# Kernel optimization log

Measured on AMD Instinct MI355X. Metric: run time of the kernel, lower is better.

Reference implementation:

```python
import jax, jax.numpy as jnp
import numpy as np

H = 8          # num_heads
D = 64         # out_dim per head
ROT = D // 2   # rotary dim per spatial axis (out_dim // relative_emb_dim)
MIN_FREQ = 1.0 / 64


def _freqs(t):
    # t: (bs, N) coordinates -> (bs, N, ROT)
    inv_freq = 1.0 / (10000.0 ** (jnp.arange(0, ROT, 2, dtype=jnp.float32) / ROT))
    f = (t / MIN_FREQ)[..., None] * inv_freq  # (bs, N, ROT/2)
    return jnp.concatenate([f, f], axis=-1)   # (bs, N, ROT)


def _rotate_half(x):
    x1, x2 = jnp.split(x, 2, axis=-1)
    return jnp.concatenate([-x2, x1], axis=-1)


def _rope(t, f):
    return t * jnp.cos(f) + _rotate_half(t) * jnp.sin(f)


def reference(h, pos, Wq, Wk, Wv, src, dst):
    bs, N, _ = pos.shape
    hb = h.reshape(bs, N, -1)                       # (bs, N, C)
    # Faithful to torch: Linear output (bs,N,H*D) .view(bs,H,N,D) is a raw
    # memory reinterpretation, i.e. a reshape, not a transpose.
    Qh = (hb @ Wq.T).reshape(bs, H, N, D)
    Kh = (hb @ Wk.T).reshape(bs, H, N, D)
    Vh = (hb @ Wv.T).reshape(bs, H, N, D)

    fx = _freqs(pos[..., 0])[:, None]               # (bs, 1, N, ROT) broadcast over heads
    fy = _freqs(pos[..., 1])[:, None]

    def rope2d(t):
        return jnp.concatenate([_rope(t[..., :ROT], fx), _rope(t[..., ROT:], fy)], axis=-1)

    Qh = rope2d(Qh)
    Kh = rope2d(Kh)

    Qn = Qh.reshape(-1, H, D)                       # (bs*N, H, D) flat node layout
    Kn = Kh.reshape(-1, H, D)
    Vn = Vh.reshape(-1, H, D)

    # edge attention: gather, dot, clamped exp, scatter-sum
    score = jnp.sum(Kn[src] * Qn[dst], axis=-1)     # (E, H)
    score = jnp.exp(jnp.clip(score / np.sqrt(D).astype(np.float32), -5.0, 5.0))

    nseg = bs * N
    wV = jax.ops.segment_sum(Vn[src] * score[..., None], dst, num_segments=nseg)  # (nseg,H,D)
    z = jax.ops.segment_sum(score, dst, num_segments=nseg)                        # (nseg,H)

    attn_out = wV / z[..., None]
    return attn_out.reshape(-1, H * D)


def setup_inputs() -> dict:
    key = jax.random.key(0)
    k = jax.random.split(key, 7)
    bs, N, C, E = 4, 4096, 256, 524288
    return {
        "h": jax.random.normal(k[0], (bs * N, C), dtype=jnp.float32),
        "pos": jax.random.uniform(k[1], (bs, N, 2), dtype=jnp.float32),
        "Wq": jax.random.normal(k[2], (H * D, C), dtype=jnp.float32) * 0.05,
        "Wk": jax.random.normal(k[3], (H * D, C), dtype=jnp.float32) * 0.05,
        "Wv": jax.random.normal(k[4], (H * D, C), dtype=jnp.float32) * 0.05,
        "src": jax.random.randint(k[5], (E,), 0, bs * N, dtype=jnp.int32),
        "dst": jax.random.randint(k[6], (E,), 0, bs * N, dtype=jnp.int32),
    }
```

## Files before the change

kernel.cpp:

```cpp
#include <hip/hip_runtime.h>
#include <math.h>

#define NODES 16384
#define CIN   256
#define HD    512
#define NPOS  4096
#define NHEAD 8
#define DDIM  64
#define HN    (NODES * CIN)
#define WN    (HD * CIN)

typedef float f32x4 __attribute__((ext_vector_type(4)));
typedef unsigned int u32x4 __attribute__((ext_vector_type(4)));
typedef short s16x8 __attribute__((ext_vector_type(8)));

__device__ inline unsigned short f2bf(float f) {
  unsigned int u = __float_as_uint(f);
  u += 0x7fffu + ((u >> 16) & 1u);
  return (unsigned short)(u >> 16);
}

__global__ __launch_bounds__(256) void conv_rank_kernel(
    const float* __restrict__ h, const float* __restrict__ wq,
    const float* __restrict__ wk, const float* __restrict__ wv,
    unsigned short* __restrict__ out,
    const int* __restrict__ dst, int* __restrict__ count,
    int* __restrict__ rank, int E) {
  int t = blockIdx.x * 256 + threadIdx.x;
  if (t < E) rank[t] = atomicAdd(&count[dst[t]], 1);

  size_t e = (size_t)t * 8;
  const float* s;
  size_t off;
  if (e < HN)               { s = h;  off = e; }
  else if (e < HN + WN)     { s = wq; off = e - HN; }
  else if (e < HN + 2 * WN) { s = wk; off = e - HN - WN; }
  else                      { s = wv; off = e - HN - 2 * WN; }
  float4 f0 = *(const float4*)(s + off);
  float4 f1 = *(const float4*)(s + off + 4);
  u32x4 o;
  o[0] = f2bf(f0.x) | ((unsigned int)f2bf(f0.y) << 16);
  o[1] = f2bf(f0.z) | ((unsigned int)f2bf(f0.w) << 16);
  o[2] = f2bf(f1.x) | ((unsigned int)f2bf(f1.y) << 16);
  o[3] = f2bf(f1.z) | ((unsigned int)f2bf(f1.w) << 16);
  *(u32x4*)(out + e) = o;
}

__global__ __launch_bounds__(256) void scan_kernel(
    const int* __restrict__ count, int* __restrict__ offset) {
  __shared__ int psum[256];
  __shared__ int pref[256];
  int t = threadIdx.x;
  int base = t * (NODES / 256);
  int s = 0;
  for (int i = 0; i < NODES / 256; ++i) s += count[base + i];
  psum[t] = s;
  __syncthreads();
  if (t < 64) {
    int a0 = psum[4 * t], a1 = psum[4 * t + 1];
    int a2 = psum[4 * t + 2], a3 = psum[4 * t + 3];
    int loc = a0 + a1 + a2 + a3;
    int sc = loc;
#pragma unroll
    for (int d = 1; d < 64; d <<= 1) {
      int v = __shfl_up(sc, d);
      if (t >= d) sc += v;
    }
    int excl = sc - loc;
    pref[4 * t]     = excl;
    pref[4 * t + 1] = excl + a0;
    pref[4 * t + 2] = excl + a0 + a1;
    pref[4 * t + 3] = excl + a0 + a1 + a2;
  }
  __syncthreads();
  int off = pref[t];
  for (int i = 0; i < NODES / 256; ++i) {
    offset[base + i] = off;
    off += count[base + i];
  }
  if (t == 255) offset[NODES] = off;
}

__global__ __launch_bounds__(256) void place_kernel(
    const int* __restrict__ src, const int* __restrict__ dst,
    const int* __restrict__ offset, const int* __restrict__ rank,
    int* __restrict__ srcs, int E) {
  int t = blockIdx.x * 256 + threadIdx.x;
  if (t < E) srcs[offset[dst[t]] + rank[t]] = src[t];
}

__global__ __launch_bounds__(256) void gemm_mfma_kernel(
    const unsigned short* __restrict__ hb,
    const unsigned short* __restrict__ wb,
    const float* __restrict__ pos,
    unsigned short* __restrict__ Qb, unsigned short* __restrict__ Kb,
    unsigned short* __restrict__ Vb) {
  const int z = blockIdx.z;
  const unsigned short* B = wb + (size_t)z * WN;
  unsigned short* C = z == 0 ? Qb : (z == 1 ? Kb : Vb);

  __shared__ __align__(16) unsigned short As[2][128 * 32];
  __shared__ __align__(16) unsigned short Bs[2][128 * 32];

  const int tid = threadIdx.x;
  const int lane = tid & 63, w = tid >> 6;
  const int row0 = blockIdx.y * 128, col0 = blockIdx.x * 128;
  const int wr = w >> 1, wc = w & 1;

  const int r_l = lane >> 2;
  const int kc = (lane & 3) * 8;

  f32x4 acc[4][4] = {};

#define STAGE(bufi, kt)                                                        \
  {                                                                            \
    _Pragma("unroll") for (int u = 0; u < 2; ++u) {                            \
      int blk = u * 4 + w;                                                     \
      int r = blk * 16 + r_l;                                                  \
      __builtin_amdgcn_global_load_lds(                                        \
          (const __attribute__((address_space(1))) void*)(hb +                 \
              (size_t)(row0 + r) * CIN + (kt) + kc),                           \
          (__attribute__((address_space(3))) void*)(&As[bufi][blk * 512]),     \
          16, 0, 0);                                                           \
      __builtin_amdgcn_global_load_lds(                                        \
          (const __attribute__((address_space(1))) void*)(B +                  \
              (size_t)(col0 + r) * CIN + (kt) + kc),                           \
          (__attribute__((address_space(3))) void*)(&Bs[bufi][blk * 512]),     \
          16, 0, 0);                                                           \
    }                                                                          \
  }

  STAGE(0, 0);
  __syncthreads();

  int cur = 0;
  for (int t = 0; t < 8; ++t) {
    if (t < 7) STAGE(cur ^ 1, (t + 1) * 32);

    s16x8 af[4], bfr[4];
#pragma unroll
    for (int mi = 0; mi < 4; ++mi)
      af[mi] = *(const s16x8*)(&As[cur][(wr * 64 + mi * 16 + (lane & 15)) * 32 + (lane >> 4) * 8]);
#pragma unroll
    for (int ni = 0; ni < 4; ++ni)
      bfr[ni] = *(const s16x8*)(&Bs[cur][(wc * 64 + ni * 16 + (lane & 15)) * 32 + (lane >> 4) * 8]);
#pragma unroll
    for (int mi = 0; mi < 4; ++mi)
#pragma unroll
      for (int ni = 0; ni < 4; ++ni)
        acc[mi][ni] = __builtin_amdgcn_mfma_f32_16x16x32_bf16(
            af[mi], bfr[ni], acc[mi][ni], 0, 0, 0);

    __syncthreads();
    cur ^= 1;
  }
#undef STAGE

  const int head = blockIdx.x * 2 + wc;
  const int cb = col0 + wc * 64 + (lane & 15);
  const float invf = exp2f(-(float)(lane & 15) * 0.83048202372184f);

#pragma unroll
  for (int mi = 0; mi < 4; ++mi) {
#pragma unroll
    for (int r = 0; r < 4; ++r) {
      int row = row0 + wr * 64 + mi * 16 + (lane >> 4) * 4 + r;
      float v0 = acc[mi][0][r], v1 = acc[mi][1][r];
      float v2 = acc[mi][2][r], v3 = acc[mi][3][r];
      if (z < 2) {
        int b = row >> 12;
        int rem = ((row & 4095) << 3) + head;
        int n = rem & (NPOS - 1);
        const float* pp = pos + ((size_t)((b << 12) + n)) * 2;
        float a0 = pp[0] * 64.0f * invf;
        float a1 = pp[1] * 64.0f * invf;
        float s0, c0, s1, c1;
        sincosf(a0, &s0, &c0);
        sincosf(a1, &s1, &c1);
        float nx0 = v0 * c0 - v1 * s0;
        float nx1 = v1 * c0 + v0 * s0;
        float ny0 = v2 * c1 - v3 * s1;
        float ny1 = v3 * c1 + v2 * s1;
        v0 = nx0; v1 = nx1; v2 = ny0; v3 = ny1;
      }
      unsigned short* cp = C + (size_t)row * HD + cb;
      cp[0]  = f2bf(v0);
      cp[16] = f2bf(v1);
      cp[32] = f2bf(v2);
      cp[48] = f2bf(v3);
    }
  }
}

__global__ __launch_bounds__(256) void node_kernel(
    const unsigned short* __restrict__ Qb, const unsigned short* __restrict__ Kb,
    const unsigned short* __restrict__ Vb,
    const int* __restrict__ srcs, const int* __restrict__ offset,
    float* __restrict__ out) {
  __shared__ float wv[4][HD];
  __shared__ float zb[4][NHEAD];
  const int n = blockIdx.x;
  const int tid = threadIdx.x;
  const int lane = tid & 63, w = tid >> 6;
  const int hh = lane >> 3, g = lane & 7;

  const int beg = offset[n], end = offset[n + 1];

  u32x4 qu = *(const u32x4*)(Qb + (size_t)n * HD + lane * 8);
  float qf[8];
#pragma unroll
  for (int j = 0; j < 4; ++j) {
    qf[2 * j]     = __uint_as_float(qu[j] << 16);
    qf[2 * j + 1] = __uint_as_float(qu[j] & 0xffff0000u);
  }

  float a[8] = {0, 0, 0, 0, 0, 0, 0, 0};
  float zacc = 0.f;

  for (int i = beg + w; i < end; i += 4) {
    int s = srcs[i];
    u32x4 ku = *(const u32x4*)(Kb + (size_t)s * HD + lane * 8);
    u32x4 vu = *(const u32x4*)(Vb + (size_t)s * HD + lane * 8);
    float dot = 0.f;
#pragma unroll
    for (int j = 0; j < 4; ++j) {
      dot += __uint_as_float(ku[j] << 16) * qf[2 * j];
      dot += __uint_as_float(ku[j] & 0xffff0000u) * qf[2 * j + 1];
    }
    dot += __shfl_xor(dot, 1);
    dot += __shfl_xor(dot, 2);
    dot += __shfl_xor(dot, 4);
    float sc = __expf(fminf(fmaxf(dot * 0.125f, -5.0f), 5.0f));
#pragma unroll
    for (int j = 0; j < 4; ++j) {
      a[2 * j]     += __uint_as_float(vu[j] << 16) * sc;
      a[2 * j + 1] += __uint_as_float(vu[j] & 0xffff0000u) * sc;
    }
    zacc += sc;
  }

  *(float4*)&wv[w][lane * 8]     = make_float4(a[0], a[1], a[2], a[3]);
  *(float4*)&wv[w][lane * 8 + 4] = make_float4(a[4], a[5], a[6], a[7]);
  if (g == 0) zb[w][hh] = zacc;
  __syncthreads();

  const int d0 = tid * 2;
  float r0 = wv[0][d0] + wv[1][d0] + wv[2][d0] + wv[3][d0];
  float r1 = wv[0][d0 + 1] + wv[1][d0 + 1] + wv[2][d0 + 1] + wv[3][d0 + 1];
  const int head = d0 >> 6;
  float zz = zb[0][head] + zb[1][head] + zb[2][head] + zb[3][head];
  float inv = 1.0f / zz;
  *(float2*)&out[(size_t)n * HD + d0] = make_float2(r0 * inv, r1 * inv);
}

extern "C" void kernel_launch(void* const* d_in, const int* in_sizes, int n_in,
                              void* d_out, int out_size, void* d_ws,
                              size_t ws_size, hipStream_t stream) {
  const float* h   = (const float*)d_in[0];
  const float* pos = (const float*)d_in[1];
  const float* Wq  = (const float*)d_in[2];
  const float* Wk  = (const float*)d_in[3];
  const float* Wv  = (const float*)d_in[4];
  const int* src   = (const int*)d_in[5];
  const int* dst   = (const int*)d_in[6];
  const int E = in_sizes[5];

  unsigned short* hb  = (unsigned short*)d_ws;
  unsigned short* wb  = hb + HN;
  unsigned short* Qb  = wb + 3 * WN;
  unsigned short* Kb  = Qb + (size_t)NODES * HD;
  unsigned short* Vb  = Kb + (size_t)NODES * HD;
  int* count  = (int*)(Vb + (size_t)NODES * HD);
  int* offset = count + NODES;
  int* rank   = offset + NODES + 1;
  int* srcs   = rank + E;
  float* out = (float*)d_out;

  hipMemsetAsync(count, 0, NODES * sizeof(int), stream);

  conv_rank_kernel<<<(HN + 3 * WN) / 8 / 256, 256, 0, stream>>>(
      h, Wq, Wk, Wv, hb, dst, count, rank, E);

  scan_kernel<<<1, 256, 0, stream>>>(count, offset);
  place_kernel<<<(E + 255) / 256, 256, 0, stream>>>(
      src, dst, offset, rank, srcs, E);

  gemm_mfma_kernel<<<dim3(HD / 128, NODES / 128, 3), 256, 0, stream>>>(
      hb, wb, pos, Qb, Kb, Vb);

  node_kernel<<<NODES, 256, 0, stream>>>(Qb, Kb, Vb, srcs, offset, out);
}
```

Before: 284.5 us.

## Store Q/K/V head-major and split node aggregation per head

The GEMM epilogue now writes Q, K and V in a head-major layout (head, node, 64), so each head's data is contiguous. The node kernel launches a 2D grid of node groups by heads, with one wave per (node, head). Two edges are handled per iteration using half-waves, which removes the shared-memory reduction and the block barrier. The aim is better cache locality, since each head's working set (16384×64 bf16) is small enough to stay resident. In exchange, edge indices and offsets are re-read once per head, and nodes with uneven edge counts cause more load imbalance and shorter per-wave loads.

```diff
diff --git a/kernel.cpp b/kernel.cpp
--- a/kernel.cpp
+++ b/kernel.cpp
@@ -157,8 +157,8 @@
 #undef STAGE
 
   const int head = blockIdx.x * 2 + wc;
-  const int cb = col0 + wc * 64 + (lane & 15);
   const float invf = exp2f(-(float)(lane & 15) * 0.83048202372184f);
+  unsigned short* Ch = C + (size_t)head * (NODES * DDIM) + (lane & 15);
 
 #pragma unroll
   for (int mi = 0; mi < 4; ++mi) {
@@ -183,7 +183,7 @@
         float ny1 = v3 * c1 + v2 * s1;
         v0 = nx0; v1 = nx1; v2 = ny0; v3 = ny1;
       }
-      unsigned short* cp = C + (size_t)row * HD + cb;
+      unsigned short* cp = Ch + (size_t)row * DDIM;
       cp[0]  = f2bf(v0);
       cp[16] = f2bf(v1);
       cp[32] = f2bf(v2);
@@ -197,60 +197,50 @@
     const unsigned short* __restrict__ Vb,
     const int* __restrict__ srcs, const int* __restrict__ offset,
     float* __restrict__ out) {
-  __shared__ float wv[4][HD];
-  __shared__ float zb[4][NHEAD];
-  const int n = blockIdx.x;
-  const int tid = threadIdx.x;
-  const int lane = tid & 63, w = tid >> 6;
-  const int hh = lane >> 3, g = lane & 7;
+  const int w = threadIdx.x >> 6, lane = threadIdx.x & 63;
+  const int n = blockIdx.x * 4 + w;
+  const int hh = blockIdx.y;
+  const int el = lane >> 5, dl = lane & 31;
+
+  const unsigned short* Qh = Qb + (size_t)hh * (NODES * DDIM);
+  const unsigned short* Kh = Kb + (size_t)hh * (NODES * DDIM);
+  const unsigned short* Vh = Vb + (size_t)hh * (NODES * DDIM);
 
   const int beg = offset[n], end = offset[n + 1];
 
-  u32x4 qu = *(const u32x4*)(Qb + (size_t)n * HD + lane * 8);
-  float qf[8];
-#pragma unroll
-  for (int j = 0; j < 4; ++j) {
-    qf[2 * j]     = __uint_as_float(qu[j] << 16);
-    qf[2 * j + 1] = __uint_as_float(qu[j] & 0xffff0000u);
-  }
-
-  float a[8] = {0, 0, 0, 0, 0, 0, 0, 0};
-  float zacc = 0.f;
-
-  for (int i = beg + w; i < end; i += 4) {
-    int s = srcs[i];
-    u32x4 ku = *(const u32x4*)(Kb + (size_t)s * HD + lane * 8);
-    u32x4 vu = *(const u32x4*)(Vb + (size_t)s * HD + lane * 8);
-    float dot = 0.f;
-#pragma unroll
-    for (int j = 0; j < 4; ++j) {
-      dot += __uint_as_float(ku[j] << 16) * qf[2 * j];
-      dot += __uint_as_float(ku[j] & 0xffff0000u) * qf[2 * j + 1];
-    }
+  unsigned int qu = __builtin_nontemporal_load(
+      (const unsigned int*)(Qh + (size_t)n * DDIM + dl * 2));
+  float q0 = __uint_as_float(qu << 16);
+  float q1 = __uint_as_float(qu & 0xffff0000u);
+
+  float a0 = 0.f, a1 = 0.f, zacc = 0.f;
+
+  for (int i = beg; i + el < end; i += 2) {
+    int s = __builtin_nontemporal_load(&srcs[i + el]);
+    unsigned int ku = *(const unsigned int*)(Kh + (size_t)s * DDIM + dl * 2);
+    float dot = __uint_as_float(ku << 16) * q0 +
+                __uint_as_float(ku & 0xffff0000u) * q1;
     dot += __shfl_xor(dot, 1);
     dot += __shfl_xor(dot, 2);
     dot += __shfl_xor(dot, 4);
+    dot += __shfl_xor(dot, 8);
+    dot += __shfl_xor(dot, 16);
     float sc = __expf(fminf(fmaxf(dot * 0.125f, -5.0f), 5.0f));
-#pragma unroll
-    for (int j = 0; j < 4; ++j) {
-      a[2 * j]     += __uint_as_float(vu[j] << 16) * sc;
-      a[2 * j + 1] += __uint_as_float(vu[j] & 0xffff0000u) * sc;
-    }
+    unsigned int vu = *(const unsigned int*)(Vh + (size_t)s * DDIM + dl * 2);
+    a0 += __uint_as_float(vu << 16) * sc;
+    a1 += __uint_as_float(vu & 0xffff0000u) * sc;
     zacc += sc;
   }
 
-  *(float4*)&wv[w][lane * 8]     = make_float4(a[0], a[1], a[2], a[3]);
-  *(float4*)&wv[w][lane * 8 + 4] = make_float4(a[4], a[5], a[6], a[7]);
-  if (g == 0) zb[w][hh] = zacc;
-  __syncthreads();
-
-  const int d0 = tid * 2;
-  float r0 = wv[0][d0] + wv[1][d0] + wv[2][d0] + wv[3][d0];
-  float r1 = wv[0][d0 + 1] + wv[1][d0 + 1] + wv[2][d0 + 1] + wv[3][d0 + 1];
-  const int head = d0 >> 6;
-  float zz = zb[0][head] + zb[1][head] + zb[2][head] + zb[3][head];
-  float inv = 1.0f / zz;
-  *(float2*)&out[(size_t)n * HD + d0] = make_float2(r0 * inv, r1 * inv);
+  a0 += __shfl_xor(a0, 32);
+  a1 += __shfl_xor(a1, 32);
+  zacc += __shfl_xor(zacc, 32);
+
+  if (lane < 32) {
+    float inv = 1.0f / zacc;
+    *(float2*)(out + (size_t)n * HD + hh * DDIM + dl * 2) =
+        make_float2(a0 * inv, a1 * inv);
+  }
 }
 
 extern "C" void kernel_launch(void* const* d_in, const int* in_sizes, int n_in,
@@ -288,5 +278,6 @@
   gemm_mfma_kernel<<<dim3(HD / 128, NODES / 128, 3), 256, 0, stream>>>(
       hb, wb, pos, Qb, Kb, Vb);
 
-  node_kernel<<<NODES, 256, 0, stream>>>(Qb, Kb, Vb, srcs, offset, out);
-}
+  node_kernel<<<dim3(NODES / 4, NHEAD), 256, 0, stream>>>(
+      Qb, Kb, Vb, srcs, offset, out);
+}
```

After: 445.9 us. 1.57x slower.

## Store Q/K/V head-major and split node aggregation per head across wavefronts

Applied to the files above, without the earlier changes.

The GEMM epilogue now writes Q, K and V in a head-major layout (head, node, 64), so each head's data is contiguous. The node kernel launches one wavefront per (node, head): 8 edges are processed in parallel with 8 lanes each, and the partial sums are reduced with shuffles instead of a shared-memory reduction and block barrier. This targets better cache locality for the gathered K/V rows within a head and removes LDS and sync overhead. In exchange it adds masked lanes for nodes whose edge counts are not multiples of 8, and the srcs indices are reloaded once per head.

```diff
diff --git a/kernel.cpp b/kernel.cpp
--- a/kernel.cpp
+++ b/kernel.cpp
@@ -157,8 +157,8 @@
 #undef STAGE
 
   const int head = blockIdx.x * 2 + wc;
-  const int cb = col0 + wc * 64 + (lane & 15);
   const float invf = exp2f(-(float)(lane & 15) * 0.83048202372184f);
+  unsigned short* Ch = C + (size_t)head * (NODES * DDIM) + (lane & 15);
 
 #pragma unroll
   for (int mi = 0; mi < 4; ++mi) {
@@ -183,7 +183,7 @@
         float ny1 = v3 * c1 + v2 * s1;
         v0 = nx0; v1 = nx1; v2 = ny0; v3 = ny1;
       }
-      unsigned short* cp = C + (size_t)row * HD + cb;
+      unsigned short* cp = Ch + (size_t)row * DDIM;
       cp[0]  = f2bf(v0);
       cp[16] = f2bf(v1);
       cp[32] = f2bf(v2);
@@ -197,16 +197,18 @@
     const unsigned short* __restrict__ Vb,
     const int* __restrict__ srcs, const int* __restrict__ offset,
     float* __restrict__ out) {
-  __shared__ float wv[4][HD];
-  __shared__ float zb[4][NHEAD];
-  const int n = blockIdx.x;
-  const int tid = threadIdx.x;
-  const int lane = tid & 63, w = tid >> 6;
-  const int hh = lane >> 3, g = lane & 7;
+  const int w = threadIdx.x >> 6, lane = threadIdx.x & 63;
+  const int n = blockIdx.x * 4 + w;
+  const int hh = blockIdx.y;
+  const int e8 = lane >> 3, d8 = lane & 7;
+
+  const unsigned short* Qh = Qb + (size_t)hh * (NODES * DDIM);
+  const unsigned short* Kh = Kb + (size_t)hh * (NODES * DDIM);
+  const unsigned short* Vh = Vb + (size_t)hh * (NODES * DDIM);
 
   const int beg = offset[n], end = offset[n + 1];
 
-  u32x4 qu = *(const u32x4*)(Qb + (size_t)n * HD + lane * 8);
+  u32x4 qu = *(const u32x4*)(Qh + (size_t)n * DDIM + d8 * 8);
   float qf[8];
 #pragma unroll
   for (int j = 0; j < 4; ++j) {
@@ -217,10 +219,12 @@
   float a[8] = {0, 0, 0, 0, 0, 0, 0, 0};
   float zacc = 0.f;
 
-  for (int i = beg + w; i < end; i += 4) {
-    int s = srcs[i];
-    u32x4 ku = *(const u32x4*)(Kb + (size_t)s * HD + lane * 8);
-    u32x4 vu = *(const u32x4*)(Vb + (size_t)s * HD + lane * 8);
+  for (int it = beg; it < end; it += 8) {
+    int e = it + e8;
+    bool ok = e < end;
+    int s = __builtin_nontemporal_load(&srcs[ok ? e : beg]);
+    u32x4 ku = *(const u32x4*)(Kh + (size_t)s * DDIM + d8 * 8);
+    u32x4 vu = *(const u32x4*)(Vh + (size_t)s * DDIM + d8 * 8);
     float dot = 0.f;
 #pragma unroll
     for (int j = 0; j < 4; ++j) {
@@ -230,7 +234,7 @@
     dot += __shfl_xor(dot, 1);
     dot += __shfl_xor(dot, 2);
     dot += __shfl_xor(dot, 4);
-    float sc = __expf(fminf(fmaxf(dot * 0.125f, -5.0f), 5.0f));
+    float sc = ok ? __expf(fminf(fmaxf(dot * 0.125f, -5.0f), 5.0f)) : 0.f;
 #pragma unroll
     for (int j = 0; j < 4; ++j) {
       a[2 * j]     += __uint_as_float(vu[j] << 16) * sc;
@@ -239,18 +243,21 @@
     zacc += sc;
   }
 
-  *(float4*)&wv[w][lane * 8]     = make_float4(a[0], a[1], a[2], a[3]);
-  *(float4*)&wv[w][lane * 8 + 4] = make_float4(a[4], a[5], a[6], a[7]);
-  if (g == 0) zb[w][hh] = zacc;
-  __syncthreads();
-
-  const int d0 = tid * 2;
-  float r0 = wv[0][d0] + wv[1][d0] + wv[2][d0] + wv[3][d0];
-  float r1 = wv[0][d0 + 1] + wv[1][d0 + 1] + wv[2][d0 + 1] + wv[3][d0 + 1];
-  const int head = d0 >> 6;
-  float zz = zb[0][head] + zb[1][head] + zb[2][head] + zb[3][head];
-  float inv = 1.0f / zz;
-  *(float2*)&out[(size_t)n * HD + d0] = make_float2(r0 * inv, r1 * inv);
+#pragma unroll
+  for (int d = 8; d < 64; d <<= 1) {
+#pragma unroll
+    for (int j = 0; j < 8; ++j) a[j] += __shfl_xor(a[j], d);
+    zacc += __shfl_xor(zacc, d);
+  }
+
+  if (e8 == 0) {
+    float inv = 1.0f / zacc;
+    float4 o0 = make_float4(a[0] * inv, a[1] * inv, a[2] * inv, a[3] * inv);
+    float4 o1 = make_float4(a[4] * inv, a[5] * inv, a[6] * inv, a[7] * inv);
+    float* op = out + (size_t)n * HD + hh * DDIM + d8 * 8;
+    *(float4*)op = o0;
+    *(float4*)(op + 4) = o1;
+  }
 }
 
 extern "C" void kernel_launch(void* const* d_in, const int* in_sizes, int n_in,
@@ -288,5 +295,6 @@
   gemm_mfma_kernel<<<dim3(HD / 128, NODES / 128, 3), 256, 0, stream>>>(
       hb, wb, pos, Qb, Kb, Vb);
 
-  node_kernel<<<NODES, 256, 0, stream>>>(Qb, Kb, Vb, srcs, offset, out);
-}
+  node_kernel<<<dim3(NODES / 4, NHEAD), 256, 0, stream>>>(
+      Qb, Kb, Vb, srcs, offset, out);
+}
```

After: 272.0 us. 4.4% less time.
